# Kernel optimization log

Hardware: AMD Instinct MI355X
Metric: run time of the kernel (lower is better)

Reference implementation:

```python
import jax, jax.numpy as jnp
import numpy as np

N = 262144   # cohort size (k_n)
M = 8192     # number of ordinal anchor indices (len(Hj))


def setup_inputs() -> dict:
    key = jax.random.key(0)
    k1, k2, k3, k4, k5 = jax.random.split(key, 5)
    time = jax.random.uniform(k1, (N,), dtype=jnp.float32) * 1000.0
    event = (jax.random.uniform(k2, (N,), dtype=jnp.float32) < 0.3).astype(jnp.float32)
    y_true0 = jnp.stack([time, event], axis=1)          # [N,2] (time, event)
    y_true1 = y_true0                                    # second head labels (unused by loss)
    y_pred0 = jax.random.normal(k3, (N, 1), dtype=jnp.float32) * 0.1  # xbeta head 0
    y_pred1 = jax.random.normal(k4, (N, 1), dtype=jnp.float32) * 0.1  # xbeta head 1
    Hj = jnp.sort(jax.random.randint(k5, (M,), 0, N, dtype=jnp.int32))  # static event indices into sorted order
    log_vars = jnp.zeros((2, 1), dtype=jnp.float32)      # layer weights log_var0, log_var1
    return {"y_true0": y_true0, "y_true1": y_true1, "y_pred0": y_pred0,
            "y_pred1": y_pred1, "Hj": Hj, "log_vars": log_vars}


def reference(y_true0, y_true1, y_pred0, y_pred1, Hj, log_vars):
    n = y_true0.shape[0]
    # top_k with k = n == full descending sort by time
    _, order = jax.lax.top_k(y_true0[:, 0], n)

    # ---- neg_log_pl (Cox negative partial log-likelihood, per-sample vector) ----
    xbeta = y_pred0[order, 0]                 # [N] sorted by descending time
    event = y_true0[order, 1]                 # [N]
    denom = jnp.cumsum(jnp.exp(xbeta))        # risk-set cumulative sum
    lossA = -(event * (xbeta - jnp.log(denom)))  # [N]

    # ---- ordinal_loss0 (pairwise ranking over event indices Hj in sorted order) ----
    # intended math: for each j, for ii >= j: cost += 1 - exp(xbeta[Hj[j]] - xbeta[Hj[ii]])
    xb = y_pred1[order, 0]                    # [N] sorted
    xh = xb[Hj]                               # [M]
    m = Hj.shape[0]
    rec = 1.0 - jnp.exp(xh[:, None] - xh[None, :])   # [M,M] rec[j,ii]
    mask = jnp.triu(jnp.ones((m, m), dtype=bool))    # ii >= j
    cost2 = jnp.sum(jnp.where(mask, rec, 0.0))

    # ---- multi_loss combination with learned log variances ----
    lv0 = log_vars[0, 0]
    lv1 = log_vars[1, 0]
    precision1 = jnp.clip(jnp.exp(-lv1), 0.0, 1.0)
    loss = jnp.sum(lossA + lv0) + (precision1 * cost2 + lv1)
    return loss


if __name__ == "__main__":
    out = reference(**setup_inputs())
    print(out)
```

## Files before the change

### kernel.cpp

```cpp
#include <hip/hip_runtime.h>
#include <math.h>


#define BSHIFT 12
#define NBUCK (1 << 19)
#define BLK 256
#define NC1 32
#define M40 ((1ull << 40) - 1)

#define STORE_U32(p, v) __hip_atomic_store((p), (v), __ATOMIC_RELAXED, __HIP_MEMORY_SCOPE_AGENT)
#define STORE_F32(p, v) __hip_atomic_store((p), (v), __ATOMIC_RELAXED, __HIP_MEMORY_SCOPE_AGENT)
#define STORE_U64(p, v) __hip_atomic_store((unsigned long long*)(p), (v), __ATOMIC_RELAXED, __HIP_MEMORY_SCOPE_AGENT)
#define LOAD_U32(p) __hip_atomic_load((p), __ATOMIC_RELAXED, __HIP_MEMORY_SCOPE_AGENT)

template <int GRID>
__device__ __forceinline__ void gbar(unsigned* bar, unsigned gv) {
  __syncthreads();
  constexpr unsigned BPC = GRID / NC1;
  const int t = threadIdx.x;
  const unsigned grp = blockIdx.x & (NC1 - 1);
  if (blockIdx.x == 0) {
    if (t == 0) {
      unsigned a = __hip_atomic_fetch_add(bar + grp * 16, 1u,
                                          __ATOMIC_RELAXED, __HIP_MEMORY_SCOPE_AGENT);
      if (a == gv * BPC - 1u) STORE_U32(bar + 512 + grp * 16, gv);
    }
    if (t < NC1) {
      int guard = 0;
      while (LOAD_U32(bar + 512 + t * 16) < gv) {
        __builtin_amdgcn_s_sleep(1);
        if (++guard > 5000000) break;
      }
      STORE_U32(bar + 1024 + t * 16, gv);
    }
    __syncthreads();
  } else {
    if (t == 0) {
      unsigned a = __hip_atomic_fetch_add(bar + grp * 16, 1u,
                                          __ATOMIC_RELAXED, __HIP_MEMORY_SCOPE_AGENT);
      if (a == gv * BPC - 1u) STORE_U32(bar + 512 + grp * 16, gv);
      int guard = 0;
      while (LOAD_U32(bar + 1024 + grp * 16) < gv) {
        __builtin_amdgcn_s_sleep(1);
        if (++guard > 5000000) break;
      }
    }
    __syncthreads();
  }
}

template <int GRID>
__global__ void __launch_bounds__(BLK, 4)
k_fused(const float2* __restrict__ yt0, const float* __restrict__ yp0,
        const float* __restrict__ yp1, const int* __restrict__ Hj,
        const float* __restrict__ lv, int n, int m,
        unsigned* __restrict__ bar,
        unsigned long long* __restrict__ rec, unsigned* __restrict__ bitmap,
        unsigned long long* __restrict__ Epack, unsigned* __restrict__ bTot,
        float* __restrict__ fTot, uint2* __restrict__ skey2,
        unsigned* __restrict__ sidx, float* __restrict__ xh,
        double* __restrict__ accum, float* __restrict__ out)
{
  constexpr int TOT = GRID * BLK;
  constexpr int BPB = NBUCK / GRID;
  constexpr int BPT = BPB / BLK;
  const int t = threadIdx.x;
  const int g = blockIdx.x;
  const int gtid = g * BLK + t;

  __shared__ unsigned su[BLK];
  __shared__ float    sff[BLK];
  __shared__ double   sd[BLK];
  __shared__ float    wt[4];

  unsigned keyR[2]; float seR[2]; unsigned seqR[2]; unsigned evR[2];
  #pragma unroll
  for (int el = 0; el < 2; ++el) {
    int i = gtid + el * TOT;
    keyR[el] = 0u; seR[el] = 0.f; seqR[el] = 0u; evR[el] = 0u;
    if (i < n) {
      float2 te = yt0[i];
      unsigned key = __float_as_uint(te.x);
      keyR[el] = key;
      evR[el] = (te.y != 0.f) ? 0x80000000u : 0u;
      float e = expf(yp0[i]);
      seR[el] = e;
      unsigned long long qe = (unsigned long long)(e * 16777216.0f + 0.5f);
      if (qe > (1ull << 32)) qe = (1ull << 32);
      unsigned long long ret =
          atomicAdd(&rec[key >> BSHIFT], (1ull << 40) | qe);
      seqR[el] = (unsigned)(ret >> 40);
    }
  }
  for (int j = gtid; j < m; j += TOT) {
    int h = Hj[j];
    atomicOr(&bitmap[h >> 5], 1u << (h & 31));
  }
  gbar<GRID>(bar, 1);

  unsigned cK[BPT]; float fK[BPT];
  unsigned thrC; float thrF;
  {
    unsigned runc = 0u; float runf = 0.f;
    #pragma unroll
    for (int k = 0; k < BPT; ++k) {
      int b = NBUCK - 1 - (g * BPB + t * BPT + k);
      unsigned long long v = rec[b];
      cK[k] = (unsigned)(v >> 40);
      fK[k] = (float)((double)(v & M40) * (1.0 / 16777216.0));
      runc += cK[k]; runf += fK[k];
    }
    su[t] = runc; sff[t] = runf;
    __syncthreads();
    for (int off2 = 1; off2 < BLK; off2 <<= 1) {
      unsigned uc = (t >= off2) ? su[t - off2] : 0u;
      float    uf = (t >= off2) ? sff[t - off2] : 0.f;
      __syncthreads();
      su[t] += uc; sff[t] += uf;
      __syncthreads();
    }
    thrC = (t > 0) ? su[t - 1] : 0u;
    thrF = (t > 0) ? sff[t - 1] : 0.f;
    if (t == BLK - 1) { STORE_U32(&bTot[g], su[t]); STORE_F32(&fTot[g], sff[t]); }
  }
  gbar<GRID>(bar, 2);

  {
    unsigned partC = 0u; float partF = 0.f;
    for (int j = t; j < g; j += BLK) { partC += bTot[j]; partF += fTot[j]; }
    su[t] = partC; sff[t] = partF;
    __syncthreads();
    for (int s = BLK / 2; s > 0; s >>= 1) {
      if (t < s) { su[t] += su[t + s]; sff[t] += sff[t + s]; }
      __syncthreads();
    }
    unsigned baseC = su[0]; float baseF = sff[0];
    __syncthreads();
    unsigned preC = 0u; float preF = 0.f;
    #pragma unroll
    for (int k = 0; k < BPT; ++k) {
      int b = NBUCK - 1 - (g * BPB + t * BPT + k);
      unsigned sfxC = baseC + thrC + preC;
      float    sfxF = baseF + thrF + preF;
      unsigned long long w =
          ((unsigned long long)__float_as_uint(sfxF) << 32) | sfxC;
      STORE_U64(&Epack[b], w);
      preC += cK[k]; preF += fK[k];
    }
  }
  gbar<GRID>(bar, 3);

  #pragma unroll
  for (int el = 0; el < 2; ++el) {
    int i = gtid + el * TOT;
    if (i < n) {
      unsigned key = keyR[el];
      unsigned b = key >> BSHIFT;
      unsigned start = ((const unsigned*)Epack)[2u * b];
      unsigned pos = start + seqR[el];
      unsigned long long v =
          ((unsigned long long)__float_as_uint(seR[el]) << 32) | key;
      STORE_U64(&skey2[pos], v);
      STORE_U32(&sidx[pos], (unsigned)i | evR[el]);
    }
  }
  gbar<GRID>(bar, 4);

  {
    double contrib = 0.0;
    #pragma unroll
    for (int el = 0; el < 2; ++el) {
      int p = gtid + el * TOT;
      if (p >= n) continue;
      uint2 kv = skey2[p];
      unsigned key = kv.x;
      float e = __uint_as_float(kv.y);
      unsigned sidv = sidx[p];
      unsigned idx = sidv & 0x7FFFFFFFu;
      bool evb = (sidv >> 31) != 0u;
      unsigned b = key >> BSHIFT;
      unsigned long long ep = Epack[b];
      unsigned start = (unsigned)ep;
      float cross = __uint_as_float((unsigned)(ep >> 32));
      unsigned end = (b > 0) ? ((const unsigned*)Epack)[2u * (b - 1)]
                             : (unsigned)n;
      if (end > (unsigned)n) end = (unsigned)n;
      if (start > end) start = end;
      float wsum = 0.f;
      unsigned wcnt = 0u;
      unsigned q = start;
      while (q + 8 <= end) {
        uint2 v[8];
        #pragma unroll
        for (int k = 0; k < 8; ++k) v[k] = skey2[q + k];
        #pragma unroll
        for (int k = 0; k < 8; ++k) {
          if (v[k].x > key) { wsum += __uint_as_float(v[k].y); wcnt++; }
          else if (v[k].x == key && (sidx[q + k] & 0x7FFFFFFFu) < idx) {
            wsum += __uint_as_float(v[k].y); wcnt++;
          }
        }
        q += 8;
      }
      for (; q < end; ++q) {
        uint2 v = skey2[q];
        if (v.x > key) { wsum += __uint_as_float(v.y); wcnt++; }
        else if (v.x == key && (sidx[q] & 0x7FFFFFFFu) < idx) {
          wsum += __uint_as_float(v.y); wcnt++;
        }
      }
      float denom = cross + wsum + e;
      int rank = (int)(start + wcnt);
      if (evb) contrib += (double)logf(denom / e);
      if ((bitmap[rank >> 5] >> (rank & 31)) & 1u) {
        int lo = 0, hi = m;
        while (lo < hi) { int mid = (lo + hi) >> 1; if (Hj[mid] < rank) lo = mid + 1; else hi = mid; }
        if (lo < m && Hj[lo] == rank) {
          float xb1 = yp1[idx];
          for (int j = lo; j < m && Hj[j] == rank; ++j) STORE_F32(&xh[j], xb1);
        }
      }
    }
    sd[t] = contrib;
    __syncthreads();
    for (int s = 128; s > 0; s >>= 1) { if (t < s) sd[t] += sd[t + s]; __syncthreads(); }
    if (t == 0) atomicAdd(accum, sd[0]);
  }
  gbar<GRID>(bar, 5);

  if (g != 0) return;
  {
    int lane = t & 63;
    int w = t >> 6;
    double acc = 0.0;
    float carry = 0.f;
    int passes = (m + 2047) / 2048;
    for (int pss = passes - 1; pss >= 0; --pss) {
      int base = pss * 2048 + t * 8;
      float x[8], eb[8];
      float c = 0.f;
      #pragma unroll
      for (int k = 0; k < 8; ++k) {
        int j = base + k;
        x[k] = (j < m) ? xh[j] : 0.f;
        eb[k] = (j < m) ? expf(-x[k]) : 0.f;
        c += eb[k];
      }
      float s = c;
      #pragma unroll
      for (int d = 1; d < 64; d <<= 1) {
        float o = __shfl_down(s, d, 64);
        if (lane + d < 64) s += o;
      }
      float wtot = __shfl(s, 0, 64);
      if (lane == 0) wt[w] = wtot;
      __syncthreads();
      float after = 0.f, ptot = 0.f;
      #pragma unroll
      for (int w2 = 0; w2 < 4; ++w2) { ptot += wt[w2]; if (w2 > w) after += wt[w2]; }
      float S = (s - c) + after + carry;
      #pragma unroll
      for (int k = 7; k >= 0; --k) {
        int j = base + k;
        S += eb[k];
        if (j < m) acc += (double)(expf(x[k]) * S);
      }
      __syncthreads();
      carry += ptot;
    }
    sd[t] = acc;
    __syncthreads();
    for (int s2 = 128; s2 > 0; s2 >>= 1) { if (t < s2) sd[t] += sd[t + s2]; __syncthreads(); }
    if (t == 0) {
      double T = (double)m * (double)(m + 1) * 0.5;
      double cost2 = T - sd[0];
      float lv0 = lv[0], lv1 = lv[1];
      float prec1 = fminf(expf(-lv1), 1.0f);
      double loss = *accum + (double)n * (double)lv0 + (double)prec1 * cost2 + (double)lv1;
      out[0] = (float)loss;
    }
  }
}

extern "C" void kernel_launch(void* const* d_in, const int* in_sizes, int n_in,
                              void* d_out, int out_size, void* d_ws, size_t ws_size,
                              hipStream_t stream) {
  (void)n_in; (void)out_size;
  const float2* yt0 = (const float2*)d_in[0];
  const float*  yp0 = (const float*)d_in[2];
  const float*  yp1 = (const float*)d_in[3];
  const int*    Hj  = (const int*)d_in[4];
  const float*  lv  = (const float*)d_in[5];
  int n = in_sizes[0] / 2;
  int m = in_sizes[4];

  char* ws = (char*)d_ws;
  unsigned* bar   = (unsigned*)ws;
  double*   accum = (double*)(ws + 7168);
  size_t off = 8192;
  auto alloc = [&](size_t bytes) -> void* {
    void* p = ws + off;
    off += (bytes + 255) & ~(size_t)255;
    return p;
  };
  size_t nbm = ((size_t)(n + 31) / 32) * 4;
  unsigned* bitmap = (unsigned*)alloc(nbm);
  unsigned long long* rec = (unsigned long long*)alloc((size_t)NBUCK * 8);
  size_t zbytes = off;
  unsigned long long* Epack = (unsigned long long*)alloc((size_t)NBUCK * 8);
  unsigned* bTot  = (unsigned*)alloc(1024 * 4);
  float*    fTot  = (float*)alloc(1024 * 4);
  uint2*    skey2 = (uint2*)alloc((size_t)n * 8);
  unsigned* sidx  = (unsigned*)alloc((size_t)n * 4);
  float*    xh    = (float*)alloc((size_t)m * 4);
  if (off > ws_size) return;

  hipMemsetAsync(ws, 0, zbytes, stream);

  static int gridChoice = 0;
  if (gridChoice == 0) {
    int nb = 0;
    hipError_t e1 = hipOccupancyMaxActiveBlocksPerMultiprocessor(&nb, k_fused<1024>, BLK, 0);
    int dev = 0; hipGetDevice(&dev);
    hipDeviceProp_t prop;
    hipError_t e2 = hipGetDeviceProperties(&prop, dev);
    gridChoice = (e1 == hipSuccess && e2 == hipSuccess &&
                  nb * prop.multiProcessorCount >= 1024) ? 1024 : 512;
  }
  if (gridChoice == 1024)
    k_fused<1024><<<dim3(1024), dim3(BLK), 0, stream>>>(
        yt0, yp0, yp1, Hj, lv, n, m, bar, rec, bitmap, Epack, bTot, fTot,
        skey2, sidx, xh, accum, (float*)d_out);
  else
    k_fused<512><<<dim3(512), dim3(BLK), 0, stream>>>(
        yt0, yp0, yp1, Hj, lv, n, m, bar, rec, bitmap, Epack, bTot, fTot,
        skey2, sidx, xh, accum, (float*)d_out);
}
```

Before: 138.3 us.

## Use per-XCD L2 writeback barrier for scatter and drop release in last barrier

```diff
diff --git a/kernel.cpp b/kernel.cpp
--- a/kernel.cpp
+++ b/kernel.cpp
@@ -8,10 +8,27 @@
 #define NC1 32
 #define M40 ((1ull << 40) - 1)
 
+#define BAR_FLAG 512
+#define BAR_REL  1024
+#define BAR_SEEN 1536
+#define BAR_DONE 1552
+#define BAR_ELECT 1568
+
 #define STORE_U32(p, v) __hip_atomic_store((p), (v), __ATOMIC_RELAXED, __HIP_MEMORY_SCOPE_AGENT)
 #define STORE_F32(p, v) __hip_atomic_store((p), (v), __ATOMIC_RELAXED, __HIP_MEMORY_SCOPE_AGENT)
 #define STORE_U64(p, v) __hip_atomic_store((unsigned long long*)(p), (v), __ATOMIC_RELAXED, __HIP_MEMORY_SCOPE_AGENT)
 #define LOAD_U32(p) __hip_atomic_load((p), __ATOMIC_RELAXED, __HIP_MEMORY_SCOPE_AGENT)
+#define FADD_U32(p, v) __hip_atomic_fetch_add((p), (v), __ATOMIC_RELAXED, __HIP_MEMORY_SCOPE_AGENT)
+#define FOR_U32(p, v) __hip_atomic_fetch_or((p), (v), __ATOMIC_RELAXED, __HIP_MEMORY_SCOPE_AGENT)
+
+__device__ __forceinline__ void l2_writeback() {
+#if __has_builtin(__builtin_amdgcn_buffer_wbl2)
+  __builtin_amdgcn_buffer_wbl2();
+  __builtin_amdgcn_s_waitcnt(0);
+#else
+  __builtin_amdgcn_fence(__ATOMIC_RELEASE, "agent");
+#endif
+}
 
 template <int GRID>
 __device__ __forceinline__ void gbar(unsigned* bar, unsigned gv) {
@@ -21,31 +38,101 @@
   const unsigned grp = blockIdx.x & (NC1 - 1);
   if (blockIdx.x == 0) {
     if (t == 0) {
-      unsigned a = __hip_atomic_fetch_add(bar + grp * 16, 1u,
-                                          __ATOMIC_RELAXED, __HIP_MEMORY_SCOPE_AGENT);
-      if (a == gv * BPC - 1u) STORE_U32(bar + 512 + grp * 16, gv);
+      unsigned a = FADD_U32(bar + grp * 16, 1u);
+      if (a == gv * BPC - 1u) STORE_U32(bar + BAR_FLAG + grp * 16, gv);
     }
     if (t < NC1) {
       int guard = 0;
-      while (LOAD_U32(bar + 512 + t * 16) < gv) {
+      while (LOAD_U32(bar + BAR_FLAG + t * 16) < gv) {
         __builtin_amdgcn_s_sleep(1);
         if (++guard > 5000000) break;
       }
-      STORE_U32(bar + 1024 + t * 16, gv);
+      STORE_U32(bar + BAR_REL + t * 16, gv);
     }
     __syncthreads();
   } else {
     if (t == 0) {
-      unsigned a = __hip_atomic_fetch_add(bar + grp * 16, 1u,
-                                          __ATOMIC_RELAXED, __HIP_MEMORY_SCOPE_AGENT);
-      if (a == gv * BPC - 1u) STORE_U32(bar + 512 + grp * 16, gv);
+      unsigned a = FADD_U32(bar + grp * 16, 1u);
+      if (a == gv * BPC - 1u) STORE_U32(bar + BAR_FLAG + grp * 16, gv);
       int guard = 0;
-      while (LOAD_U32(bar + 1024 + grp * 16) < gv) {
+      while (LOAD_U32(bar + BAR_REL + grp * 16) < gv) {
         __builtin_amdgcn_s_sleep(1);
         if (++guard > 5000000) break;
       }
     }
     __syncthreads();
+  }
+}
+
+template <int GRID>
+__device__ __forceinline__ void gbar_flush(unsigned* bar, unsigned gv) {
+  __syncthreads();
+  constexpr unsigned BPC = GRID / NC1;
+  const int t = threadIdx.x;
+  const unsigned grp = blockIdx.x & (NC1 - 1);
+  if (t == 0) {
+    unsigned xcd = __builtin_amdgcn_s_getreg((3 << 11) | 20) & 7u;
+    FOR_U32(bar + BAR_SEEN, 1u << xcd);
+    bool flusher = (FADD_U32(bar + BAR_ELECT + xcd * 16, 1u) == 0u);
+    unsigned a = FADD_U32(bar + grp * 16, 1u);
+    if (a == gv * BPC - 1u) STORE_U32(bar + BAR_FLAG + grp * 16, gv);
+    if (blockIdx.x == 0) {
+      int guard = 0; unsigned ok = 0;
+      while (ok < NC1) {
+        ok = 0;
+        #pragma unroll
+        for (int i = 0; i < NC1; ++i)
+          ok += (LOAD_U32(bar + BAR_FLAG + i * 16) >= gv) ? 1u : 0u;
+        if (ok < NC1) __builtin_amdgcn_s_sleep(1);
+        if (++guard > 2000000) break;
+      }
+      #pragma unroll
+      for (int i = 0; i < NC1; ++i) STORE_U32(bar + BAR_REL + i * 16, gv);
+    } else {
+      int guard = 0;
+      while (LOAD_U32(bar + BAR_REL + grp * 16) < gv) {
+        __builtin_amdgcn_s_sleep(1);
+        if (++guard > 5000000) break;
+      }
+    }
+    if (flusher) {
+      l2_writeback();
+      FOR_U32(bar + BAR_DONE, 1u << xcd);
+    }
+    unsigned sm = LOAD_U32(bar + BAR_SEEN);
+    int guard = 0;
+    while ((LOAD_U32(bar + BAR_DONE) & sm) != sm) {
+      __builtin_amdgcn_s_sleep(1);
+      if (++guard > 5000000) break;
+    }
+  }
+  __syncthreads();
+}
+
+template <int GRID>
+__device__ __forceinline__ void gbar_last(unsigned* bar, unsigned gv) {
+  __syncthreads();
+  constexpr unsigned BPC = GRID / NC1;
+  const int t = threadIdx.x;
+  const unsigned grp = blockIdx.x & (NC1 - 1);
+  if (blockIdx.x == 0) {
+    if (t == 0) {
+      unsigned a = FADD_U32(bar + grp * 16, 1u);
+      if (a == gv * BPC - 1u) STORE_U32(bar + BAR_FLAG + grp * 16, gv);
+    }
+    if (t < NC1) {
+      int guard = 0;
+      while (LOAD_U32(bar + BAR_FLAG + t * 16) < gv) {
+        __builtin_amdgcn_s_sleep(1);
+        if (++guard > 5000000) break;
+      }
+    }
+    __syncthreads();
+  } else {
+    if (t == 0) {
+      unsigned a = FADD_U32(bar + grp * 16, 1u);
+      if (a == gv * BPC - 1u) STORE_U32(bar + BAR_FLAG + grp * 16, gv);
+    }
   }
 }
 
@@ -158,13 +245,12 @@
       unsigned b = key >> BSHIFT;
       unsigned start = ((const unsigned*)Epack)[2u * b];
       unsigned pos = start + seqR[el];
-      unsigned long long v =
-          ((unsigned long long)__float_as_uint(seR[el]) << 32) | key;
-      STORE_U64(&skey2[pos], v);
-      STORE_U32(&sidx[pos], (unsigned)i | evR[el]);
-    }
-  }
-  gbar<GRID>(bar, 4);
+      uint2 v; v.x = key; v.y = __float_as_uint(seR[el]);
+      skey2[pos] = v;
+      sidx[pos] = (unsigned)i | evR[el];
+    }
+  }
+  gbar_flush<GRID>(bar, 4);
 
   {
     double contrib = 0.0;
@@ -226,7 +312,7 @@
     for (int s = 128; s > 0; s >>= 1) { if (t < s) sd[t] += sd[t + s]; __syncthreads(); }
     if (t == 0) atomicAdd(accum, sd[0]);
   }
-  gbar<GRID>(bar, 5);
+  gbar_last<GRID>(bar, 5);
 
   if (g != 0) return;
   {
@@ -296,8 +382,8 @@
 
   char* ws = (char*)d_ws;
   unsigned* bar   = (unsigned*)ws;
-  double*   accum = (double*)(ws + 7168);
-  size_t off = 8192;
+  double*   accum = (double*)(ws + 15360);
+  size_t off = 16384;
   auto alloc = [&](size_t bytes) -> void* {
     void* p = ws + off;
     off += (bytes + 255) & ~(size_t)255;
```

Result: slower. 149.4 us (+8.0%).

## Split fused persistent kernel into histogram, scan and main kernels

Applied to the files above, without the earlier changes.

```diff
diff --git a/kernel.cpp b/kernel.cpp
--- a/kernel.cpp
+++ b/kernel.cpp
@@ -8,10 +8,14 @@
 #define NC1 32
 #define M40 ((1ull << 40) - 1)
 
+#define BAR_FLAG 512
+#define BAR_REL  1024
+
 #define STORE_U32(p, v) __hip_atomic_store((p), (v), __ATOMIC_RELAXED, __HIP_MEMORY_SCOPE_AGENT)
 #define STORE_F32(p, v) __hip_atomic_store((p), (v), __ATOMIC_RELAXED, __HIP_MEMORY_SCOPE_AGENT)
 #define STORE_U64(p, v) __hip_atomic_store((unsigned long long*)(p), (v), __ATOMIC_RELAXED, __HIP_MEMORY_SCOPE_AGENT)
 #define LOAD_U32(p) __hip_atomic_load((p), __ATOMIC_RELAXED, __HIP_MEMORY_SCOPE_AGENT)
+#define FADD_U32(p, v) __hip_atomic_fetch_add((p), (v), __ATOMIC_RELAXED, __HIP_MEMORY_SCOPE_AGENT)
 
 template <int GRID>
 __device__ __forceinline__ void gbar(unsigned* bar, unsigned gv) {
@@ -21,26 +25,24 @@
   const unsigned grp = blockIdx.x & (NC1 - 1);
   if (blockIdx.x == 0) {
     if (t == 0) {
-      unsigned a = __hip_atomic_fetch_add(bar + grp * 16, 1u,
-                                          __ATOMIC_RELAXED, __HIP_MEMORY_SCOPE_AGENT);
-      if (a == gv * BPC - 1u) STORE_U32(bar + 512 + grp * 16, gv);
+      unsigned a = FADD_U32(bar + grp * 16, 1u);
+      if (a == gv * BPC - 1u) STORE_U32(bar + BAR_FLAG + grp * 16, gv);
     }
     if (t < NC1) {
       int guard = 0;
-      while (LOAD_U32(bar + 512 + t * 16) < gv) {
+      while (LOAD_U32(bar + BAR_FLAG + t * 16) < gv) {
         __builtin_amdgcn_s_sleep(1);
         if (++guard > 5000000) break;
       }
-      STORE_U32(bar + 1024 + t * 16, gv);
+      STORE_U32(bar + BAR_REL + t * 16, gv);
     }
     __syncthreads();
   } else {
     if (t == 0) {
-      unsigned a = __hip_atomic_fetch_add(bar + grp * 16, 1u,
-                                          __ATOMIC_RELAXED, __HIP_MEMORY_SCOPE_AGENT);
-      if (a == gv * BPC - 1u) STORE_U32(bar + 512 + grp * 16, gv);
+      unsigned a = FADD_U32(bar + grp * 16, 1u);
+      if (a == gv * BPC - 1u) STORE_U32(bar + BAR_FLAG + grp * 16, gv);
       int guard = 0;
-      while (LOAD_U32(bar + 1024 + grp * 16) < gv) {
+      while (LOAD_U32(bar + BAR_REL + grp * 16) < gv) {
         __builtin_amdgcn_s_sleep(1);
         if (++guard > 5000000) break;
       }
@@ -50,17 +52,53 @@
 }
 
 template <int GRID>
+__device__ __forceinline__ void gbar_last(unsigned* bar, unsigned gv) {
+  __syncthreads();
+  constexpr unsigned BPC = GRID / NC1;
+  const int t = threadIdx.x;
+  const unsigned grp = blockIdx.x & (NC1 - 1);
+  if (blockIdx.x == 0) {
+    if (t == 0) {
+      unsigned a = FADD_U32(bar + grp * 16, 1u);
+      if (a == gv * BPC - 1u) STORE_U32(bar + BAR_FLAG + grp * 16, gv);
+    }
+    if (t < NC1) {
+      int guard = 0;
+      while (LOAD_U32(bar + BAR_FLAG + t * 16) < gv) {
+        __builtin_amdgcn_s_sleep(1);
+        if (++guard > 5000000) break;
+      }
+    }
+    __syncthreads();
+  } else {
+    if (t == 0) {
+      unsigned a = FADD_U32(bar + grp * 16, 1u);
+      if (a == gv * BPC - 1u) STORE_U32(bar + BAR_FLAG + grp * 16, gv);
+    }
+  }
+}
+
 __global__ void __launch_bounds__(BLK, 4)
-k_fused(const float2* __restrict__ yt0, const float* __restrict__ yp0,
-        const float* __restrict__ yp1, const int* __restrict__ Hj,
-        const float* __restrict__ lv, int n, int m,
-        unsigned* __restrict__ bar,
-        unsigned long long* __restrict__ rec, unsigned* __restrict__ bitmap,
-        unsigned long long* __restrict__ Epack, unsigned* __restrict__ bTot,
-        float* __restrict__ fTot, uint2* __restrict__ skey2,
-        unsigned* __restrict__ sidx, float* __restrict__ xh,
-        double* __restrict__ accum, float* __restrict__ out)
-{
+k_hist(const float2* __restrict__ yt0, const float* __restrict__ yp0, int n,
+       unsigned long long* __restrict__ rec, unsigned* __restrict__ seq) {
+  int i = blockIdx.x * BLK + threadIdx.x;
+  if (i >= n) return;
+  float2 te = yt0[i];
+  unsigned key = __float_as_uint(te.x);
+  float e = expf(yp0[i]);
+  unsigned long long qe = (unsigned long long)(e * 16777216.0f + 0.5f);
+  if (qe > (1ull << 32)) qe = (1ull << 32);
+  unsigned long long ret = atomicAdd(&rec[key >> BSHIFT], (1ull << 40) | qe);
+  seq[i] = (unsigned)(ret >> 40);
+}
+
+template <int GRID>
+__global__ void __launch_bounds__(BLK, 4)
+k_scan(const unsigned long long* __restrict__ rec,
+       const int* __restrict__ Hj, int m,
+       unsigned* __restrict__ bar, unsigned* __restrict__ bitmap,
+       unsigned long long* __restrict__ Epack,
+       unsigned* __restrict__ bTot, float* __restrict__ fTot) {
   constexpr int TOT = GRID * BLK;
   constexpr int BPB = NBUCK / GRID;
   constexpr int BPT = BPB / BLK;
@@ -70,33 +108,11 @@
 
   __shared__ unsigned su[BLK];
   __shared__ float    sff[BLK];
-  __shared__ double   sd[BLK];
-  __shared__ float    wt[4];
-
-  unsigned keyR[2]; float seR[2]; unsigned seqR[2]; unsigned evR[2];
-  #pragma unroll
-  for (int el = 0; el < 2; ++el) {
-    int i = gtid + el * TOT;
-    keyR[el] = 0u; seR[el] = 0.f; seqR[el] = 0u; evR[el] = 0u;
-    if (i < n) {
-      float2 te = yt0[i];
-      unsigned key = __float_as_uint(te.x);
-      keyR[el] = key;
-      evR[el] = (te.y != 0.f) ? 0x80000000u : 0u;
-      float e = expf(yp0[i]);
-      seR[el] = e;
-      unsigned long long qe = (unsigned long long)(e * 16777216.0f + 0.5f);
-      if (qe > (1ull << 32)) qe = (1ull << 32);
-      unsigned long long ret =
-          atomicAdd(&rec[key >> BSHIFT], (1ull << 40) | qe);
-      seqR[el] = (unsigned)(ret >> 40);
-    }
-  }
+
   for (int j = gtid; j < m; j += TOT) {
     int h = Hj[j];
     atomicOr(&bitmap[h >> 5], 1u << (h & 31));
   }
-  gbar<GRID>(bar, 1);
 
   unsigned cK[BPT]; float fK[BPT];
   unsigned thrC; float thrF;
@@ -123,7 +139,7 @@
     thrF = (t > 0) ? sff[t - 1] : 0.f;
     if (t == BLK - 1) { STORE_U32(&bTot[g], su[t]); STORE_F32(&fTot[g], sff[t]); }
   }
-  gbar<GRID>(bar, 2);
+  gbar<GRID>(bar, 1);
 
   {
     unsigned partC = 0u; float partF = 0.f;
@@ -142,29 +158,49 @@
       int b = NBUCK - 1 - (g * BPB + t * BPT + k);
       unsigned sfxC = baseC + thrC + preC;
       float    sfxF = baseF + thrF + preF;
-      unsigned long long w =
-          ((unsigned long long)__float_as_uint(sfxF) << 32) | sfxC;
-      STORE_U64(&Epack[b], w);
+      Epack[b] = ((unsigned long long)__float_as_uint(sfxF) << 32) | sfxC;
       preC += cK[k]; preF += fK[k];
     }
   }
-  gbar<GRID>(bar, 3);
+}
+
+template <int GRID>
+__global__ void __launch_bounds__(BLK, 4)
+k_main(const float2* __restrict__ yt0, const float* __restrict__ yp0,
+       const float* __restrict__ yp1, const int* __restrict__ Hj,
+       const float* __restrict__ lv, int n, int m,
+       unsigned* __restrict__ bar, const unsigned* __restrict__ seq,
+       const unsigned* __restrict__ bitmap,
+       const unsigned long long* __restrict__ Epack,
+       uint2* __restrict__ skey2, unsigned* __restrict__ sidx,
+       float* __restrict__ xh, double* __restrict__ accum,
+       float* __restrict__ out) {
+  constexpr int TOT = GRID * BLK;
+  const int t = threadIdx.x;
+  const int g = blockIdx.x;
+  const int gtid = g * BLK + t;
+
+  __shared__ double sd[BLK];
+  __shared__ float  wt[4];
 
   #pragma unroll
   for (int el = 0; el < 2; ++el) {
     int i = gtid + el * TOT;
     if (i < n) {
-      unsigned key = keyR[el];
+      float2 te = yt0[i];
+      unsigned key = __float_as_uint(te.x);
+      unsigned ev = (te.y != 0.f) ? 0x80000000u : 0u;
+      float e = expf(yp0[i]);
       unsigned b = key >> BSHIFT;
       unsigned start = ((const unsigned*)Epack)[2u * b];
-      unsigned pos = start + seqR[el];
+      unsigned pos = start + seq[i];
       unsigned long long v =
-          ((unsigned long long)__float_as_uint(seR[el]) << 32) | key;
+          ((unsigned long long)__float_as_uint(e) << 32) | key;
       STORE_U64(&skey2[pos], v);
-      STORE_U32(&sidx[pos], (unsigned)i | evR[el]);
-    }
-  }
-  gbar<GRID>(bar, 4);
+      STORE_U32(&sidx[pos], (unsigned)i | ev);
+    }
+  }
+  gbar<GRID>(bar, 1);
 
   {
     double contrib = 0.0;
@@ -226,7 +262,7 @@
     for (int s = 128; s > 0; s >>= 1) { if (t < s) sd[t] += sd[t + s]; __syncthreads(); }
     if (t == 0) atomicAdd(accum, sd[0]);
   }
-  gbar<GRID>(bar, 5);
+  gbar_last<GRID>(bar, 2);
 
   if (g != 0) return;
   {
@@ -295,9 +331,10 @@
   int m = in_sizes[4];
 
   char* ws = (char*)d_ws;
-  unsigned* bar   = (unsigned*)ws;
-  double*   accum = (double*)(ws + 7168);
-  size_t off = 8192;
+  unsigned* barS  = (unsigned*)ws;
+  unsigned* barM  = (unsigned*)(ws + 8192);
+  double*   accum = (double*)(ws + 16128);
+  size_t off = 16384;
   auto alloc = [&](size_t bytes) -> void* {
     void* p = ws + off;
     off += (bytes + 255) & ~(size_t)255;
@@ -310,6 +347,7 @@
   unsigned long long* Epack = (unsigned long long*)alloc((size_t)NBUCK * 8);
   unsigned* bTot  = (unsigned*)alloc(1024 * 4);
   float*    fTot  = (float*)alloc(1024 * 4);
+  unsigned* seq   = (unsigned*)alloc((size_t)n * 4);
   uint2*    skey2 = (uint2*)alloc((size_t)n * 8);
   unsigned* sidx  = (unsigned*)alloc((size_t)n * 4);
   float*    xh    = (float*)alloc((size_t)m * 4);
@@ -320,19 +358,29 @@
   static int gridChoice = 0;
   if (gridChoice == 0) {
     int nb = 0;
-    hipError_t e1 = hipOccupancyMaxActiveBlocksPerMultiprocessor(&nb, k_fused<1024>, BLK, 0);
+    hipError_t e1 = hipOccupancyMaxActiveBlocksPerMultiprocessor(&nb, k_main<1024>, BLK, 0);
     int dev = 0; hipGetDevice(&dev);
     hipDeviceProp_t prop;
     hipError_t e2 = hipGetDeviceProperties(&prop, dev);
     gridChoice = (e1 == hipSuccess && e2 == hipSuccess &&
                   nb * prop.multiProcessorCount >= 1024) ? 1024 : 512;
   }
-  if (gridChoice == 1024)
-    k_fused<1024><<<dim3(1024), dim3(BLK), 0, stream>>>(
-        yt0, yp0, yp1, Hj, lv, n, m, bar, rec, bitmap, Epack, bTot, fTot,
-        skey2, sidx, xh, accum, (float*)d_out);
-  else
-    k_fused<512><<<dim3(512), dim3(BLK), 0, stream>>>(
-        yt0, yp0, yp1, Hj, lv, n, m, bar, rec, bitmap, Epack, bTot, fTot,
-        skey2, sidx, xh, accum, (float*)d_out);
-}
+
+  int gHist = (n + BLK - 1) / BLK;
+  k_hist<<<dim3(gHist), dim3(BLK), 0, stream>>>(yt0, yp0, n, rec, seq);
+  if (gridChoice == 1024) {
+    k_scan<1024><<<dim3(1024), dim3(BLK), 0, stream>>>(rec, Hj, m, barS, bitmap,
+                                                       Epack, bTot, fTot);
+    k_main<1024><<<dim3(1024), dim3(BLK), 0, stream>>>(yt0, yp0, yp1, Hj, lv, n, m,
+                                                       barM, seq, bitmap, Epack,
+                                                       skey2, sidx, xh, accum,
+                                                       (float*)d_out);
+  } else {
+    k_scan<512><<<dim3(512), dim3(BLK), 0, stream>>>(rec, Hj, m, barS, bitmap,
+                                                     Epack, bTot, fTot);
+    k_main<512><<<dim3(512), dim3(BLK), 0, stream>>>(yt0, yp0, yp1, Hj, lv, n, m,
+                                                     barM, seq, bitmap, Epack,
+                                                     skey2, sidx, xh, accum,
+                                                     (float*)d_out);
+  }
+}
```

Result: no change. 136.5 us (-1.3%).

## Split persistent fused kernel into multi-kernel pipeline with linear time buckets

Applied to the files above, without the earlier changes.

```diff
diff --git a/kernel.cpp b/kernel.cpp
--- a/kernel.cpp
+++ b/kernel.cpp
@@ -2,283 +2,242 @@
 #include <math.h>
 
 
-#define BSHIFT 12
-#define NBUCK (1 << 19)
+#define NB (1 << 20)
 #define BLK 256
-#define NC1 32
 #define M40 ((1ull << 40) - 1)
 
-#define STORE_U32(p, v) __hip_atomic_store((p), (v), __ATOMIC_RELAXED, __HIP_MEMORY_SCOPE_AGENT)
-#define STORE_F32(p, v) __hip_atomic_store((p), (v), __ATOMIC_RELAXED, __HIP_MEMORY_SCOPE_AGENT)
-#define STORE_U64(p, v) __hip_atomic_store((unsigned long long*)(p), (v), __ATOMIC_RELAXED, __HIP_MEMORY_SCOPE_AGENT)
-#define LOAD_U32(p) __hip_atomic_load((p), __ATOMIC_RELAXED, __HIP_MEMORY_SCOPE_AGENT)
-
-template <int GRID>
-__device__ __forceinline__ void gbar(unsigned* bar, unsigned gv) {
-  __syncthreads();
-  constexpr unsigned BPC = GRID / NC1;
-  const int t = threadIdx.x;
-  const unsigned grp = blockIdx.x & (NC1 - 1);
-  if (blockIdx.x == 0) {
-    if (t == 0) {
-      unsigned a = __hip_atomic_fetch_add(bar + grp * 16, 1u,
-                                          __ATOMIC_RELAXED, __HIP_MEMORY_SCOPE_AGENT);
-      if (a == gv * BPC - 1u) STORE_U32(bar + 512 + grp * 16, gv);
-    }
-    if (t < NC1) {
-      int guard = 0;
-      while (LOAD_U32(bar + 512 + t * 16) < gv) {
-        __builtin_amdgcn_s_sleep(1);
-        if (++guard > 5000000) break;
-      }
-      STORE_U32(bar + 1024 + t * 16, gv);
-    }
-    __syncthreads();
-  } else {
-    if (t == 0) {
-      unsigned a = __hip_atomic_fetch_add(bar + grp * 16, 1u,
-                                          __ATOMIC_RELAXED, __HIP_MEMORY_SCOPE_AGENT);
-      if (a == gv * BPC - 1u) STORE_U32(bar + 512 + grp * 16, gv);
-      int guard = 0;
-      while (LOAD_U32(bar + 1024 + grp * 16) < gv) {
-        __builtin_amdgcn_s_sleep(1);
-        if (++guard > 5000000) break;
-      }
-    }
-    __syncthreads();
-  }
-}
-
-template <int GRID>
-__global__ void __launch_bounds__(BLK, 4)
-k_fused(const float2* __restrict__ yt0, const float* __restrict__ yp0,
-        const float* __restrict__ yp1, const int* __restrict__ Hj,
-        const float* __restrict__ lv, int n, int m,
-        unsigned* __restrict__ bar,
-        unsigned long long* __restrict__ rec, unsigned* __restrict__ bitmap,
-        unsigned long long* __restrict__ Epack, unsigned* __restrict__ bTot,
-        float* __restrict__ fTot, uint2* __restrict__ skey2,
-        unsigned* __restrict__ sidx, float* __restrict__ xh,
-        double* __restrict__ accum, float* __restrict__ out)
-{
-  constexpr int TOT = GRID * BLK;
-  constexpr int BPB = NBUCK / GRID;
-  constexpr int BPT = BPB / BLK;
-  const int t = threadIdx.x;
-  const int g = blockIdx.x;
-  const int gtid = g * BLK + t;
-
-  __shared__ unsigned su[BLK];
-  __shared__ float    sff[BLK];
-  __shared__ double   sd[BLK];
-  __shared__ float    wt[4];
-
-  unsigned keyR[2]; float seR[2]; unsigned seqR[2]; unsigned evR[2];
-  #pragma unroll
-  for (int el = 0; el < 2; ++el) {
-    int i = gtid + el * TOT;
-    keyR[el] = 0u; seR[el] = 0.f; seqR[el] = 0u; evR[el] = 0u;
-    if (i < n) {
-      float2 te = yt0[i];
-      unsigned key = __float_as_uint(te.x);
-      keyR[el] = key;
-      evR[el] = (te.y != 0.f) ? 0x80000000u : 0u;
-      float e = expf(yp0[i]);
-      seR[el] = e;
-      unsigned long long qe = (unsigned long long)(e * 16777216.0f + 0.5f);
-      if (qe > (1ull << 32)) qe = (1ull << 32);
-      unsigned long long ret =
-          atomicAdd(&rec[key >> BSHIFT], (1ull << 40) | qe);
-      seqR[el] = (unsigned)(ret >> 40);
-    }
-  }
-  for (int j = gtid; j < m; j += TOT) {
+__device__ __forceinline__ int lin_bucket(float t) {
+  int b = (int)(t * 1024.0f);
+  if (b < 0) b = 0;
+  if (b > NB - 1) b = NB - 1;
+  return b;
+}
+
+__global__ void __launch_bounds__(BLK, 4)
+k_hist(const float2* __restrict__ yt0, const float* __restrict__ yp0,
+       const int* __restrict__ Hj, int n, int m, int tot,
+       unsigned long long* __restrict__ rec, unsigned* __restrict__ seq,
+       uint2* __restrict__ ke, unsigned* __restrict__ bitmap) {
+  int i = blockIdx.x * BLK + threadIdx.x;
+  if (i < n) {
+    float2 te = yt0[i];
+    unsigned key = __float_as_uint(te.x);
+    unsigned ev = (te.y != 0.f) ? 0x80000000u : 0u;
+    float e = expf(yp0[i]);
+    int b = lin_bucket(te.x);
+    unsigned long long qe = (unsigned long long)(e * 16777216.0f + 0.5f);
+    if (qe > (1ull << 32)) qe = (1ull << 32);
+    unsigned long long ret = atomicAdd(&rec[b], (1ull << 40) | qe);
+    seq[i] = (unsigned)(ret >> 40);
+    uint2 kv; kv.x = key; kv.y = __float_as_uint(e) | ev;
+    ke[i] = kv;
+  }
+  for (int j = i; j < m; j += tot) {
     int h = Hj[j];
     atomicOr(&bitmap[h >> 5], 1u << (h & 31));
   }
-  gbar<GRID>(bar, 1);
-
-  unsigned cK[BPT]; float fK[BPT];
-  unsigned thrC; float thrF;
-  {
-    unsigned runc = 0u; float runf = 0.f;
-    #pragma unroll
-    for (int k = 0; k < BPT; ++k) {
-      int b = NBUCK - 1 - (g * BPB + t * BPT + k);
-      unsigned long long v = rec[b];
-      cK[k] = (unsigned)(v >> 40);
-      fK[k] = (float)((double)(v & M40) * (1.0 / 16777216.0));
-      runc += cK[k]; runf += fK[k];
-    }
-    su[t] = runc; sff[t] = runf;
-    __syncthreads();
-    for (int off2 = 1; off2 < BLK; off2 <<= 1) {
-      unsigned uc = (t >= off2) ? su[t - off2] : 0u;
-      float    uf = (t >= off2) ? sff[t - off2] : 0.f;
-      __syncthreads();
-      su[t] += uc; sff[t] += uf;
-      __syncthreads();
-    }
-    thrC = (t > 0) ? su[t - 1] : 0u;
-    thrF = (t > 0) ? sff[t - 1] : 0.f;
-    if (t == BLK - 1) { STORE_U32(&bTot[g], su[t]); STORE_F32(&fTot[g], sff[t]); }
-  }
-  gbar<GRID>(bar, 2);
-
-  {
-    unsigned partC = 0u; float partF = 0.f;
-    for (int j = t; j < g; j += BLK) { partC += bTot[j]; partF += fTot[j]; }
-    su[t] = partC; sff[t] = partF;
-    __syncthreads();
-    for (int s = BLK / 2; s > 0; s >>= 1) {
-      if (t < s) { su[t] += su[t + s]; sff[t] += sff[t + s]; }
-      __syncthreads();
-    }
-    unsigned baseC = su[0]; float baseF = sff[0];
-    __syncthreads();
-    unsigned preC = 0u; float preF = 0.f;
-    #pragma unroll
-    for (int k = 0; k < BPT; ++k) {
-      int b = NBUCK - 1 - (g * BPB + t * BPT + k);
-      unsigned sfxC = baseC + thrC + preC;
-      float    sfxF = baseF + thrF + preF;
-      unsigned long long w =
-          ((unsigned long long)__float_as_uint(sfxF) << 32) | sfxC;
-      STORE_U64(&Epack[b], w);
-      preC += cK[k]; preF += fK[k];
-    }
-  }
-  gbar<GRID>(bar, 3);
-
+}
+
+__global__ void __launch_bounds__(BLK, 4)
+k_scanA(const unsigned long long* __restrict__ rec,
+        unsigned* __restrict__ bTot, float* __restrict__ fTot) {
+  __shared__ unsigned su[BLK];
+  __shared__ float    sf[BLK];
+  const int t = threadIdx.x, g = blockIdx.x;
+  unsigned c = 0u; float f = 0.f;
   #pragma unroll
-  for (int el = 0; el < 2; ++el) {
-    int i = gtid + el * TOT;
-    if (i < n) {
-      unsigned key = keyR[el];
-      unsigned b = key >> BSHIFT;
-      unsigned start = ((const unsigned*)Epack)[2u * b];
-      unsigned pos = start + seqR[el];
-      unsigned long long v =
-          ((unsigned long long)__float_as_uint(seR[el]) << 32) | key;
-      STORE_U64(&skey2[pos], v);
-      STORE_U32(&sidx[pos], (unsigned)i | evR[el]);
-    }
-  }
-  gbar<GRID>(bar, 4);
-
-  {
-    double contrib = 0.0;
-    #pragma unroll
-    for (int el = 0; el < 2; ++el) {
-      int p = gtid + el * TOT;
-      if (p >= n) continue;
-      uint2 kv = skey2[p];
-      unsigned key = kv.x;
-      float e = __uint_as_float(kv.y);
-      unsigned sidv = sidx[p];
-      unsigned idx = sidv & 0x7FFFFFFFu;
-      bool evb = (sidv >> 31) != 0u;
-      unsigned b = key >> BSHIFT;
-      unsigned long long ep = Epack[b];
-      unsigned start = (unsigned)ep;
-      float cross = __uint_as_float((unsigned)(ep >> 32));
-      unsigned end = (b > 0) ? ((const unsigned*)Epack)[2u * (b - 1)]
-                             : (unsigned)n;
-      if (end > (unsigned)n) end = (unsigned)n;
-      if (start > end) start = end;
-      float wsum = 0.f;
-      unsigned wcnt = 0u;
-      unsigned q = start;
-      while (q + 8 <= end) {
-        uint2 v[8];
-        #pragma unroll
-        for (int k = 0; k < 8; ++k) v[k] = skey2[q + k];
-        #pragma unroll
-        for (int k = 0; k < 8; ++k) {
-          if (v[k].x > key) { wsum += __uint_as_float(v[k].y); wcnt++; }
-          else if (v[k].x == key && (sidx[q + k] & 0x7FFFFFFFu) < idx) {
-            wsum += __uint_as_float(v[k].y); wcnt++;
-          }
-        }
-        q += 8;
-      }
-      for (; q < end; ++q) {
+  for (int k = 0; k < 4; ++k) {
+    int b = NB - 1 - (g * 1024 + t * 4 + k);
+    unsigned long long v = rec[b];
+    c += (unsigned)(v >> 40);
+    f += (float)((double)(v & M40) * (1.0 / 16777216.0));
+  }
+  su[t] = c; sf[t] = f;
+  __syncthreads();
+  for (int s = 128; s > 0; s >>= 1) {
+    if (t < s) { su[t] += su[t + s]; sf[t] += sf[t + s]; }
+    __syncthreads();
+  }
+  if (t == 0) { bTot[g] = su[0]; fTot[g] = sf[0]; }
+}
+
+__global__ void __launch_bounds__(BLK, 4)
+k_scanB(const unsigned long long* __restrict__ rec,
+        const unsigned* __restrict__ bTot, const float* __restrict__ fTot,
+        unsigned long long* __restrict__ Epack) {
+  __shared__ unsigned su[BLK];
+  __shared__ float    sf[BLK];
+  const int t = threadIdx.x, g = blockIdx.x;
+  unsigned pc = 0u; float pf = 0.f;
+  for (int j = t; j < g; j += BLK) { pc += bTot[j]; pf += fTot[j]; }
+  su[t] = pc; sf[t] = pf;
+  __syncthreads();
+  for (int s = 128; s > 0; s >>= 1) {
+    if (t < s) { su[t] += su[t + s]; sf[t] += sf[t + s]; }
+    __syncthreads();
+  }
+  const unsigned baseC = su[0]; const float baseF = sf[0];
+  __syncthreads();
+
+  unsigned cK[4]; float fK[4];
+  unsigned runc = 0u; float runf = 0.f;
+  #pragma unroll
+  for (int k = 0; k < 4; ++k) {
+    int b = NB - 1 - (g * 1024 + t * 4 + k);
+    unsigned long long v = rec[b];
+    cK[k] = (unsigned)(v >> 40);
+    fK[k] = (float)((double)(v & M40) * (1.0 / 16777216.0));
+    runc += cK[k]; runf += fK[k];
+  }
+  su[t] = runc; sf[t] = runf;
+  __syncthreads();
+  for (int off2 = 1; off2 < BLK; off2 <<= 1) {
+    unsigned uc = (t >= off2) ? su[t - off2] : 0u;
+    float    uf = (t >= off2) ? sf[t - off2] : 0.f;
+    __syncthreads();
+    su[t] += uc; sf[t] += uf;
+    __syncthreads();
+  }
+  unsigned thrC = (t > 0) ? su[t - 1] : 0u;
+  float    thrF = (t > 0) ? sf[t - 1] : 0.f;
+  unsigned preC = 0u; float preF = 0.f;
+  #pragma unroll
+  for (int k = 0; k < 4; ++k) {
+    int b = NB - 1 - (g * 1024 + t * 4 + k);
+    unsigned sfxC = baseC + thrC + preC;
+    float    sfxF = baseF + thrF + preF;
+    Epack[b] = ((unsigned long long)__float_as_uint(sfxF) << 32) | sfxC;
+    preC += cK[k]; preF += fK[k];
+  }
+}
+
+__global__ void __launch_bounds__(BLK, 4)
+k_scatter(const uint2* __restrict__ ke, const unsigned* __restrict__ seq, int n,
+          const unsigned long long* __restrict__ Epack,
+          uint2* __restrict__ skey2, unsigned* __restrict__ sidx) {
+  int i = blockIdx.x * BLK + threadIdx.x;
+  if (i >= n) return;
+  uint2 kv = ke[i];
+  unsigned key = kv.x;
+  int b = lin_bucket(__uint_as_float(key));
+  const unsigned* E32 = (const unsigned*)Epack;
+  unsigned start = E32[2u * (unsigned)b];
+  unsigned end = (b > 0) ? E32[2u * (unsigned)(b - 1)] : (unsigned)n;
+  if (end - start < 2u) return;
+  unsigned pos = start + seq[i];
+  uint2 s; s.x = key; s.y = kv.y & 0x7FFFFFFFu;
+  skey2[pos] = s;
+  sidx[pos] = (unsigned)i;
+}
+
+__global__ void __launch_bounds__(BLK, 4)
+k_main(const uint2* __restrict__ ke, const float* __restrict__ yp1,
+       const int* __restrict__ Hj, int n, int m,
+       const unsigned* __restrict__ bitmap,
+       const unsigned long long* __restrict__ Epack,
+       const uint2* __restrict__ skey2, const unsigned* __restrict__ sidx,
+       float* __restrict__ xh, double* __restrict__ accum) {
+  __shared__ double sd[BLK];
+  const int t = threadIdx.x;
+  int i = blockIdx.x * BLK + t;
+  double contrib = 0.0;
+  if (i < n) {
+    uint2 kv = ke[i];
+    unsigned key = kv.x;
+    bool evb = (kv.y >> 31) != 0u;
+    float e = __uint_as_float(kv.y & 0x7FFFFFFFu);
+    int b = lin_bucket(__uint_as_float(key));
+    unsigned long long ep = Epack[b];
+    unsigned start = (unsigned)ep;
+    float cross = __uint_as_float((unsigned)(ep >> 32));
+    unsigned end = (b > 0) ? ((const unsigned*)Epack)[2u * (unsigned)(b - 1)]
+                           : (unsigned)n;
+    if (end > (unsigned)n) end = (unsigned)n;
+    if (start > end) start = end;
+    float wsum = 0.f;
+    unsigned wcnt = 0u;
+    if (end - start > 1u) {
+      for (unsigned q = start; q < end; ++q) {
         uint2 v = skey2[q];
         if (v.x > key) { wsum += __uint_as_float(v.y); wcnt++; }
-        else if (v.x == key && (sidx[q] & 0x7FFFFFFFu) < idx) {
+        else if (v.x == key && sidx[q] < (unsigned)i) {
           wsum += __uint_as_float(v.y); wcnt++;
         }
       }
-      float denom = cross + wsum + e;
-      int rank = (int)(start + wcnt);
-      if (evb) contrib += (double)logf(denom / e);
-      if ((bitmap[rank >> 5] >> (rank & 31)) & 1u) {
-        int lo = 0, hi = m;
-        while (lo < hi) { int mid = (lo + hi) >> 1; if (Hj[mid] < rank) lo = mid + 1; else hi = mid; }
-        if (lo < m && Hj[lo] == rank) {
-          float xb1 = yp1[idx];
-          for (int j = lo; j < m && Hj[j] == rank; ++j) STORE_F32(&xh[j], xb1);
-        }
+    }
+    float denom = cross + wsum + e;
+    int rank = (int)(start + wcnt);
+    if (evb) contrib = (double)logf(denom / e);
+    if ((bitmap[rank >> 5] >> (rank & 31)) & 1u) {
+      int lo = 0, hi = m;
+      while (lo < hi) { int mid = (lo + hi) >> 1; if (Hj[mid] < rank) lo = mid + 1; else hi = mid; }
+      if (lo < m && Hj[lo] == rank) {
+        float xb1 = yp1[i];
+        for (int j = lo; j < m && Hj[j] == rank; ++j) xh[j] = xb1;
       }
     }
-    sd[t] = contrib;
-    __syncthreads();
-    for (int s = 128; s > 0; s >>= 1) { if (t < s) sd[t] += sd[t + s]; __syncthreads(); }
-    if (t == 0) atomicAdd(accum, sd[0]);
-  }
-  gbar<GRID>(bar, 5);
-
-  if (g != 0) return;
-  {
-    int lane = t & 63;
-    int w = t >> 6;
-    double acc = 0.0;
-    float carry = 0.f;
-    int passes = (m + 2047) / 2048;
-    for (int pss = passes - 1; pss >= 0; --pss) {
-      int base = pss * 2048 + t * 8;
-      float x[8], eb[8];
-      float c = 0.f;
-      #pragma unroll
-      for (int k = 0; k < 8; ++k) {
-        int j = base + k;
-        x[k] = (j < m) ? xh[j] : 0.f;
-        eb[k] = (j < m) ? expf(-x[k]) : 0.f;
-        c += eb[k];
-      }
-      float s = c;
-      #pragma unroll
-      for (int d = 1; d < 64; d <<= 1) {
-        float o = __shfl_down(s, d, 64);
-        if (lane + d < 64) s += o;
-      }
-      float wtot = __shfl(s, 0, 64);
-      if (lane == 0) wt[w] = wtot;
-      __syncthreads();
-      float after = 0.f, ptot = 0.f;
-      #pragma unroll
-      for (int w2 = 0; w2 < 4; ++w2) { ptot += wt[w2]; if (w2 > w) after += wt[w2]; }
-      float S = (s - c) + after + carry;
-      #pragma unroll
-      for (int k = 7; k >= 0; --k) {
-        int j = base + k;
-        S += eb[k];
-        if (j < m) acc += (double)(expf(x[k]) * S);
-      }
-      __syncthreads();
-      carry += ptot;
-    }
-    sd[t] = acc;
-    __syncthreads();
-    for (int s2 = 128; s2 > 0; s2 >>= 1) { if (t < s2) sd[t] += sd[t + s2]; __syncthreads(); }
-    if (t == 0) {
-      double T = (double)m * (double)(m + 1) * 0.5;
-      double cost2 = T - sd[0];
-      float lv0 = lv[0], lv1 = lv[1];
-      float prec1 = fminf(expf(-lv1), 1.0f);
-      double loss = *accum + (double)n * (double)lv0 + (double)prec1 * cost2 + (double)lv1;
-      out[0] = (float)loss;
-    }
+  }
+  sd[t] = contrib;
+  __syncthreads();
+  for (int s = 128; s > 0; s >>= 1) { if (t < s) sd[t] += sd[t + s]; __syncthreads(); }
+  if (t == 0) atomicAdd(accum, sd[0]);
+}
+
+__global__ void __launch_bounds__(1024, 1)
+k_final(const float* __restrict__ xh, int m, int n,
+        const double* __restrict__ accum, const float* __restrict__ lv,
+        float* __restrict__ out) {
+  __shared__ float  wt[16];
+  __shared__ double dred[1024];
+  const int t = threadIdx.x;
+  int lane = t & 63;
+  int w = t >> 6;
+  double acc = 0.0;
+  float carry = 0.f;
+  int passes = (m + 8191) / 8192;
+  for (int pss = passes - 1; pss >= 0; --pss) {
+    int base = pss * 8192 + t * 8;
+    float x[8], eb[8];
+    float c = 0.f;
+    #pragma unroll
+    for (int k = 0; k < 8; ++k) {
+      int j = base + k;
+      x[k] = (j < m) ? xh[j] : 0.f;
+      eb[k] = (j < m) ? expf(-x[k]) : 0.f;
+      c += eb[k];
+    }
+    float s = c;
+    #pragma unroll
+    for (int d = 1; d < 64; d <<= 1) {
+      float o = __shfl_down(s, d, 64);
+      if (lane + d < 64) s += o;
+    }
+    float wtot = __shfl(s, 0, 64);
+    if (lane == 0) wt[w] = wtot;
+    __syncthreads();
+    float after = 0.f, ptot = 0.f;
+    #pragma unroll
+    for (int w2 = 0; w2 < 16; ++w2) { ptot += wt[w2]; if (w2 > w) after += wt[w2]; }
+    float S = (s - c) + after + carry;
+    #pragma unroll
+    for (int k = 7; k >= 0; --k) {
+      int j = base + k;
+      S += eb[k];
+      if (j < m) acc += (double)(expf(x[k]) * S);
+    }
+    __syncthreads();
+    carry += ptot;
+  }
+  dred[t] = acc;
+  __syncthreads();
+  for (int s2 = 512; s2 > 0; s2 >>= 1) { if (t < s2) dred[t] += dred[t + s2]; __syncthreads(); }
+  if (t == 0) {
+    double T = (double)m * (double)(m + 1) * 0.5;
+    double cost2 = T - dred[0];
+    float lv0 = lv[0], lv1 = lv[1];
+    float prec1 = fminf(expf(-lv1), 1.0f);
+    double loss = *accum + (double)n * (double)lv0 + (double)prec1 * cost2 + (double)lv1;
+    out[0] = (float)loss;
   }
 }
 
@@ -295,21 +254,22 @@
   int m = in_sizes[4];
 
   char* ws = (char*)d_ws;
-  unsigned* bar   = (unsigned*)ws;
-  double*   accum = (double*)(ws + 7168);
-  size_t off = 8192;
+  size_t off = 0;
   auto alloc = [&](size_t bytes) -> void* {
     void* p = ws + off;
     off += (bytes + 255) & ~(size_t)255;
     return p;
   };
+  double*   accum  = (double*)alloc(256);
   size_t nbm = ((size_t)(n + 31) / 32) * 4;
   unsigned* bitmap = (unsigned*)alloc(nbm);
-  unsigned long long* rec = (unsigned long long*)alloc((size_t)NBUCK * 8);
+  unsigned long long* rec = (unsigned long long*)alloc((size_t)NB * 8);
   size_t zbytes = off;
-  unsigned long long* Epack = (unsigned long long*)alloc((size_t)NBUCK * 8);
+  unsigned long long* Epack = (unsigned long long*)alloc((size_t)NB * 8);
   unsigned* bTot  = (unsigned*)alloc(1024 * 4);
   float*    fTot  = (float*)alloc(1024 * 4);
+  unsigned* seq   = (unsigned*)alloc((size_t)n * 4);
+  uint2*    ke    = (uint2*)alloc((size_t)n * 8);
   uint2*    skey2 = (uint2*)alloc((size_t)n * 8);
   unsigned* sidx  = (unsigned*)alloc((size_t)n * 4);
   float*    xh    = (float*)alloc((size_t)m * 4);
@@ -317,22 +277,15 @@
 
   hipMemsetAsync(ws, 0, zbytes, stream);
 
-  static int gridChoice = 0;
-  if (gridChoice == 0) {
-    int nb = 0;
-    hipError_t e1 = hipOccupancyMaxActiveBlocksPerMultiprocessor(&nb, k_fused<1024>, BLK, 0);
-    int dev = 0; hipGetDevice(&dev);
-    hipDeviceProp_t prop;
-    hipError_t e2 = hipGetDeviceProperties(&prop, dev);
-    gridChoice = (e1 == hipSuccess && e2 == hipSuccess &&
-                  nb * prop.multiProcessorCount >= 1024) ? 1024 : 512;
-  }
-  if (gridChoice == 1024)
-    k_fused<1024><<<dim3(1024), dim3(BLK), 0, stream>>>(
-        yt0, yp0, yp1, Hj, lv, n, m, bar, rec, bitmap, Epack, bTot, fTot,
-        skey2, sidx, xh, accum, (float*)d_out);
-  else
-    k_fused<512><<<dim3(512), dim3(BLK), 0, stream>>>(
-        yt0, yp0, yp1, Hj, lv, n, m, bar, rec, bitmap, Epack, bTot, fTot,
-        skey2, sidx, xh, accum, (float*)d_out);
-}
+  int gN = (n + BLK - 1) / BLK;
+  int tot = gN * BLK;
+  k_hist<<<dim3(gN), dim3(BLK), 0, stream>>>(yt0, yp0, Hj, n, m, tot,
+                                             rec, seq, ke, bitmap);
+  k_scanA<<<dim3(NB / 1024), dim3(BLK), 0, stream>>>(rec, bTot, fTot);
+  k_scanB<<<dim3(NB / 1024), dim3(BLK), 0, stream>>>(rec, bTot, fTot, Epack);
+  k_scatter<<<dim3(gN), dim3(BLK), 0, stream>>>(ke, seq, n, Epack, skey2, sidx);
+  k_main<<<dim3(gN), dim3(BLK), 0, stream>>>(ke, yp1, Hj, n, m, bitmap, Epack,
+                                             skey2, sidx, xh, accum);
+  k_final<<<dim3(1), dim3(1024), 0, stream>>>(xh, m, n, accum, lv,
+                                              (float*)d_out);
+}
```

Result: faster. 129.5 us (-6.4%).
